# Optimization experiments

Hardware: AMD Instinct MI355X
Metric: run time of the kernel (lower is better)

The kernel has to match this reference:

```python
import jax, jax.numpy as jnp
import numpy as np

N_EXPERTS = 8
TOP_K = 2


def setup_inputs() -> dict:
    key = jax.random.key(0)
    ks = jax.random.split(key, 5)
    B, T, C, E, H = 8, 2048, 256, 8, 682  # H = int(8/3*256)
    scale = 1.0 / np.sqrt(C)
    return {
        "x": jax.random.normal(ks[0], (B, T, C), dtype=jnp.float32),
        "router_w": jax.random.normal(ks[1], (E, C), dtype=jnp.float32) * scale,
        "w1": jax.random.normal(ks[2], (E, H, C), dtype=jnp.float32) * scale,
        "w2": jax.random.normal(ks[3], (E, C, H), dtype=jnp.float32) * (1.0 / np.sqrt(H)),
        "w3": jax.random.normal(ks[4], (E, H, C), dtype=jnp.float32) * scale,
    }


def reference(x, router_w, w1, w2, w3):
    B, T, C = x.shape
    flat = x.reshape(-1, C)  # [N, C]

    # Router: softmax over experts, top-k selection, renormalize.
    logits = flat @ router_w.T                     # [N, E]
    probs = jax.nn.softmax(logits, axis=-1)
    topk_probs, topk_idx = jax.lax.top_k(probs, TOP_K)
    topk_probs = topk_probs / (jnp.sum(topk_probs, axis=-1, keepdims=True) + 1e-9)

    # Dense gate matrix [N, E]: zero for non-selected experts (same math as
    # the masked loop, since unselected experts contribute weight 0).
    onehot = jax.nn.one_hot(topk_idx, N_EXPERTS, dtype=flat.dtype)  # [N, K, E]
    gates = jnp.einsum("nk,nke->ne", topk_probs, onehot)           # [N, E]

    # SwiGLU experts, computed densely over E and combined with gates.
    h1 = jnp.einsum("nc,ehc->neh", flat, w1)       # [N, E, H]
    h3 = jnp.einsum("nc,ehc->neh", flat, w3)       # [N, E, H]
    h = jax.nn.silu(h1) * h3                       # [N, E, H]
    y = jnp.einsum("neh,ech->nec", h, w2)          # [N, E, C]
    out = jnp.einsum("ne,nec->nc", gates, y)       # [N, C]
    return out.reshape(B, T, C)
```

## Files before the change

kernel.cpp:

```cpp
#include <hip/hip_runtime.h>
#include <hip/hip_bf16.h>

#define N_TOK 16384
#define C_DIM 256
#define E_NUM 8
#define H_DIM 682
#define H_PAD 768
#define NROWS (N_TOK * 2)
#define HB 64
#define APB (NROWS / HB)

typedef short short8 __attribute__((ext_vector_type(8)));
typedef float floatx4 __attribute__((ext_vector_type(4)));
typedef unsigned int uint;

__device__ inline unsigned short f2bf(float v) {
    union { float f; uint u; } x; x.f = v;
    uint r = (x.u + 0x7fffu + ((x.u >> 16) & 1u)) >> 16;
    return (unsigned short)r;
}
__device__ inline float bf2f(unsigned short v) {
    union { uint u; float f; } x; x.u = ((uint)v) << 16; return x.f;
}

__device__ __forceinline__ void load_lds16(const void* g, void* l) {
    __builtin_amdgcn_global_load_lds(
        (const __attribute__((address_space(1))) unsigned int*)g,
        (__attribute__((address_space(3))) unsigned int*)l, 16, 0, 0);
}

#define P13 (E_NUM * H_PAD * (C_DIM / 2))
#define P2  (E_NUM * C_DIM * (H_PAD / 2))
__global__ void wconvert(const float* __restrict__ w1, const float* __restrict__ w3,
                         const float* __restrict__ w2, unsigned short* __restrict__ w1b,
                         unsigned short* __restrict__ w3b, unsigned short* __restrict__ w2b) {
    int idx = blockIdx.x * 256 + threadIdx.x;
    if (idx < 2 * P13) {
        const float* src = (idx < P13) ? w1 : w3;
        unsigned short* dst = (idx < P13) ? w1b : w3b;
        int i = (idx < P13) ? idx : idx - P13;
        int e = i / (H_PAD * (C_DIM / 2));
        int rem = i - e * (H_PAD * (C_DIM / 2));
        int r = rem / (C_DIM / 2);
        int c2 = rem - r * (C_DIM / 2);
        uint v = 0;
        if (r < H_DIM) {
            const float2 f = *(const float2*)(src + ((size_t)e * H_DIM + r) * C_DIM + c2 * 2);
            v = (uint)f2bf(f.x) | ((uint)f2bf(f.y) << 16);
        }
        ((uint*)dst)[i] = v;
    } else if (idx < 2 * P13 + P2) {
        int i = idx - 2 * P13;
        int e = i / (C_DIM * (H_PAD / 2));
        int rem = i - e * (C_DIM * (H_PAD / 2));
        int r = rem / (H_PAD / 2);
        int c2 = rem - r * (H_PAD / 2);
        uint v = 0;
        if (c2 * 2 < H_DIM) {
            const float2 f = *(const float2*)(w2 + ((size_t)e * C_DIM + r) * H_DIM + c2 * 2);
            v = (uint)f2bf(f.x) | ((uint)f2bf(f.y) << 16);
        }
        ((uint*)w2b)[i] = v;
    }
}

__global__ __launch_bounds__(256) void router_kernel(
    const float* __restrict__ x, const float* __restrict__ rw,
    unsigned short* __restrict__ xb, int* __restrict__ as_e, float* __restrict__ as_gate) {
    __shared__ float rws[E_NUM * C_DIM];
    int tid = threadIdx.x;
    for (int i = tid; i < E_NUM * C_DIM; i += 256) rws[i] = rw[i];
    __syncthreads();
    int wave = tid >> 6, lane = tid & 63;
    int t = blockIdx.x * 4 + wave;
    const float4 xv = *(const float4*)(x + (size_t)t * C_DIM + lane * 4);
    uint2 pk;
    pk.x = (uint)f2bf(xv.x) | ((uint)f2bf(xv.y) << 16);
    pk.y = (uint)f2bf(xv.z) | ((uint)f2bf(xv.w) << 16);
    *(uint2*)(xb + (size_t)t * C_DIM + lane * 4) = pk;
    float p[E_NUM];
#pragma unroll
    for (int e = 0; e < E_NUM; e++) {
        const float* wr = &rws[e * C_DIM + lane * 4];
        p[e] = xv.x * wr[0] + xv.y * wr[1] + xv.z * wr[2] + xv.w * wr[3];
    }
#pragma unroll
    for (int off = 32; off >= 1; off >>= 1) {
#pragma unroll
        for (int e = 0; e < E_NUM; e++) p[e] += __shfl_down(p[e], off, 64);
    }
    if (lane == 0) {
        float m = p[0];
#pragma unroll
        for (int e = 1; e < E_NUM; e++) m = fmaxf(m, p[e]);
        float s = 0.f, q[E_NUM];
#pragma unroll
        for (int e = 0; e < E_NUM; e++) { q[e] = expf(p[e] - m); s += q[e]; }
#pragma unroll
        for (int e = 0; e < E_NUM; e++) q[e] /= s;
        int e0 = 0;
#pragma unroll
        for (int e = 1; e < E_NUM; e++) if (q[e] > q[e0]) e0 = e;
        int e1 = (e0 == 0) ? 1 : 0;
#pragma unroll
        for (int e = 0; e < E_NUM; e++) {
            if (e != e0 && q[e] > q[e1]) e1 = e;
        }
        float g0 = q[e0], g1 = q[e1];
        float denom = g0 + g1 + 1e-9f;
        g0 /= denom; g1 /= denom;
        as_e[t * 2] = e0; as_gate[t * 2] = g0;
        as_e[t * 2 + 1] = e1; as_gate[t * 2 + 1] = g1;
    }
}

__global__ __launch_bounds__(256) void hist_kernel(const int* __restrict__ as_e,
                                                   int* __restrict__ block_hist) {
    __shared__ int lh[E_NUM];
    int b = blockIdx.x, tid = threadIdx.x;
    if (tid < E_NUM) lh[tid] = 0;
    __syncthreads();
    for (int i = tid; i < APB; i += 256) atomicAdd(&lh[as_e[b * APB + i]], 1);
    __syncthreads();
    if (tid < E_NUM) block_hist[b * E_NUM + tid] = lh[tid];
}

__global__ void scan2_kernel(const int* __restrict__ block_hist, int* __restrict__ offsets,
                             int* __restrict__ block_base) {
    __shared__ int tot[E_NUM], off[E_NUM];
    int e = threadIdx.x;
    if (e < E_NUM) {
        int s = 0;
        for (int b = 0; b < HB; b++) s += block_hist[b * E_NUM + e];
        tot[e] = s;
    }
    __syncthreads();
    if (e == 0) {
        int acc = 0;
        for (int i = 0; i < E_NUM; i++) { off[i] = acc; offsets[i] = acc; acc += tot[i]; }
        offsets[E_NUM] = acc;
    }
    __syncthreads();
    if (e < E_NUM) {
        int acc = off[e];
        for (int b = 0; b < HB; b++) { block_base[b * E_NUM + e] = acc; acc += block_hist[b * E_NUM + e]; }
    }
}

__global__ __launch_bounds__(256) void scatter_kernel(
    const int* __restrict__ as_e, const int* __restrict__ block_base,
    int* __restrict__ row_token, int* __restrict__ as_row) {
    __shared__ int cur[E_NUM];
    int b = blockIdx.x, tid = threadIdx.x;
    if (tid < E_NUM) cur[tid] = block_base[b * E_NUM + tid];
    __syncthreads();
    for (int i = tid; i < APB; i += 256) {
        int a = b * APB + i;
        int e = as_e[a];
        int p = atomicAdd(&cur[e], 1);
        row_token[p] = a >> 1;
        as_row[a] = p;
    }
}

__global__ __launch_bounds__(256, 2) void expert_ffn1(
    const unsigned short* __restrict__ xb, const unsigned short* __restrict__ w1b,
    const unsigned short* __restrict__ w3b, const int* __restrict__ offsets,
    const int* __restrict__ row_token, unsigned short* __restrict__ h) {
    int e = blockIdx.x >> 6;
    int mt = blockIdx.x & 63;
    int c = blockIdx.y;
    int off0 = offsets[e], off1 = offsets[e + 1];
    int row0 = off0 + mt * 128;
    if (row0 >= off1) return;
    int mval = min(128, off1 - row0);

    __shared__ union {
        unsigned short buf[2][12288];
        unsigned short Hs[128 * 136];
    } sm;

    int tid = threadIdx.x, lane = tid & 63, w = tid >> 6;
    int wm = w & 1, wn = w >> 1;
    int ra = tid >> 2;
    int acol = (tid & 3) * 8;
    int tok0 = row_token[row0 + min(ra, mval - 1)];
    int tok1 = row_token[row0 + min(ra + 64, mval - 1)];
    const unsigned short* a0p = xb + (size_t)tok0 * C_DIM + acol;
    const unsigned short* a1p = xb + (size_t)tok1 * C_DIM + acol;
    const unsigned short* b1p0 = w1b + ((size_t)e * H_PAD + c * 128 + ra) * C_DIM + acol;
    const unsigned short* b1p1 = b1p0 + (size_t)64 * C_DIM;
    const unsigned short* b3p0 = w3b + ((size_t)e * H_PAD + c * 128 + ra) * C_DIM + acol;
    const unsigned short* b3p1 = b3p0 + (size_t)64 * C_DIM;

    int wofs = w * 512;
    auto stage = [&](int kt, int s) {
        int kb = kt * 32;
        unsigned short* base = sm.buf[s];
        load_lds16(a0p + kb, base + wofs);
        load_lds16(a1p + kb, base + 2048 + wofs);
        load_lds16(b1p0 + kb, base + 4096 + wofs);
        load_lds16(b1p1 + kb, base + 6144 + wofs);
        load_lds16(b3p0 + kb, base + 8192 + wofs);
        load_lds16(b3p1 + kb, base + 10240 + wofs);
    };

    int ko = (lane >> 4) * 8;
    int l15 = lane & 15;
    int arowf = wm * 64 + l15;
    int browf = wn * 64 + l15;
    int quad = lane >> 4;

    stage(0, 0);

    floatx4 acc1[4][4], acc3[4][4];
#pragma unroll
    for (int m = 0; m < 4; m++)
#pragma unroll
        for (int n = 0; n < 4; n++) {
            acc1[m][n] = (floatx4){0.f, 0.f, 0.f, 0.f};
            acc3[m][n] = (floatx4){0.f, 0.f, 0.f, 0.f};
        }

    for (int kt = 0; kt < 8; kt++) {
        __syncthreads();
        if (kt + 1 < 8) stage(kt + 1, (kt + 1) & 1);
        const unsigned short* cur = sm.buf[kt & 1];
        short8 af[4], b1f[4], b3f[4];
#pragma unroll
        for (int m = 0; m < 4; m++) af[m] = *(short8*)&cur[(arowf + m * 16) * 32 + ko];
#pragma unroll
        for (int n = 0; n < 4; n++) {
            b1f[n] = *(short8*)&cur[4096 + (browf + n * 16) * 32 + ko];
            b3f[n] = *(short8*)&cur[8192 + (browf + n * 16) * 32 + ko];
        }
#pragma unroll
        for (int m = 0; m < 4; m++)
#pragma unroll
            for (int n = 0; n < 4; n++) {
                acc1[m][n] = __builtin_amdgcn_mfma_f32_16x16x32_bf16(af[m], b1f[n], acc1[m][n], 0, 0, 0);
                acc3[m][n] = __builtin_amdgcn_mfma_f32_16x16x32_bf16(af[m], b3f[n], acc3[m][n], 0, 0, 0);
            }
    }
    __syncthreads();

#pragma unroll
    for (int m = 0; m < 4; m++)
#pragma unroll
        for (int n = 0; n < 4; n++)
#pragma unroll
            for (int r = 0; r < 4; r++) {
                float h1 = acc1[m][n][r], h3 = acc3[m][n][r];
                float sv = h1 / (1.0f + __expf(-h1)) * h3;
                sm.Hs[(wm * 64 + m * 16 + quad * 4 + r) * 136 + wn * 64 + n * 16 + l15] = f2bf(sv);
            }
    __syncthreads();
#pragma unroll
    for (int it = 0; it < 8; it++) {
        int s = it * 256 + tid;
        int row = s >> 4, c16 = s & 15;
        if (row < mval)
            *(int4*)(h + (size_t)(row0 + row) * H_PAD + c * 128 + c16 * 8) =
                *(int4*)&sm.Hs[row * 136 + c16 * 8];
    }
}

__global__ __launch_bounds__(256, 2) void expert_ffn2(
    const unsigned short* __restrict__ h, const unsigned short* __restrict__ w2b,
    const int* __restrict__ offsets, unsigned short* __restrict__ y) {
    int e = blockIdx.x >> 6;
    int mt = blockIdx.x & 63;
    int p = blockIdx.y;
    int off0 = offsets[e], off1 = offsets[e + 1];
    int row0 = off0 + mt * 128;
    if (row0 >= off1) return;
    int mval = min(128, off1 - row0);

    __shared__ union {
        unsigned short buf[2][8192];
        unsigned short Hs[128 * 136];
    } sm;

    int tid = threadIdx.x, lane = tid & 63, w = tid >> 6;
    int wm = w & 1, wn = w >> 1;
    int ra = tid >> 2;
    int acol = (tid & 3) * 8;
    const unsigned short* ap0 = h + (size_t)(row0 + ra) * H_PAD + acol;
    const unsigned short* ap1 = ap0 + (size_t)64 * H_PAD;
    const unsigned short* bp0 = w2b + ((size_t)e * C_DIM + p * 128 + ra) * H_PAD + acol;
    const unsigned short* bp1 = bp0 + (size_t)64 * H_PAD;

    int wofs = w * 512;
    auto stage = [&](int kt, int s) {
        int kb = kt * 32;
        unsigned short* base = sm.buf[s];
        load_lds16(ap0 + kb, base + wofs);
        load_lds16(ap1 + kb, base + 2048 + wofs);
        load_lds16(bp0 + kb, base + 4096 + wofs);
        load_lds16(bp1 + kb, base + 6144 + wofs);
    };

    int ko = (lane >> 4) * 8;
    int l15 = lane & 15;
    int arowf = wm * 64 + l15;
    int browf = wn * 64 + l15;
    int quad = lane >> 4;

    stage(0, 0);

    floatx4 acc[4][4];
#pragma unroll
    for (int m = 0; m < 4; m++)
#pragma unroll
        for (int n = 0; n < 4; n++) acc[m][n] = (floatx4){0.f, 0.f, 0.f, 0.f};

    for (int kt = 0; kt < H_PAD / 32; kt++) {
        __syncthreads();
        if (kt + 1 < H_PAD / 32) stage(kt + 1, (kt + 1) & 1);
        const unsigned short* cur = sm.buf[kt & 1];
        short8 af[4], bf[4];
#pragma unroll
        for (int m = 0; m < 4; m++) af[m] = *(short8*)&cur[(arowf + m * 16) * 32 + ko];
#pragma unroll
        for (int n = 0; n < 4; n++) bf[n] = *(short8*)&cur[4096 + (browf + n * 16) * 32 + ko];
#pragma unroll
        for (int m = 0; m < 4; m++)
#pragma unroll
            for (int n = 0; n < 4; n++)
                acc[m][n] = __builtin_amdgcn_mfma_f32_16x16x32_bf16(af[m], bf[n], acc[m][n], 0, 0, 0);
    }
    __syncthreads();

#pragma unroll
    for (int m = 0; m < 4; m++)
#pragma unroll
        for (int n = 0; n < 4; n++)
#pragma unroll
            for (int r = 0; r < 4; r++)
                sm.Hs[(wm * 64 + m * 16 + quad * 4 + r) * 136 + wn * 64 + n * 16 + l15] =
                    f2bf(acc[m][n][r]);
    __syncthreads();
#pragma unroll
    for (int it = 0; it < 8; it++) {
        int s = it * 256 + tid;
        int row = s >> 4, c16 = s & 15;
        if (row < mval)
            *(int4*)(y + (size_t)(row0 + row) * C_DIM + p * 128 + c16 * 8) =
                *(int4*)&sm.Hs[row * 136 + c16 * 8];
    }
}

__global__ __launch_bounds__(256) void combine_kernel(
    const unsigned short* __restrict__ y, const int* __restrict__ as_row,
    const float* __restrict__ as_gate, float* __restrict__ out) {
    int tid = threadIdx.x, lane = tid & 63;
    int t = blockIdx.x * 4 + (tid >> 6);
    int r0 = as_row[2 * t], r1 = as_row[2 * t + 1];
    float g0 = as_gate[2 * t], g1 = as_gate[2 * t + 1];
    uint2 a = *(const uint2*)(y + (size_t)r0 * C_DIM + lane * 4);
    uint2 b = *(const uint2*)(y + (size_t)r1 * C_DIM + lane * 4);
    float4 o;
    o.x = g0 * bf2f((unsigned short)(a.x & 0xffff)) + g1 * bf2f((unsigned short)(b.x & 0xffff));
    o.y = g0 * bf2f((unsigned short)(a.x >> 16)) + g1 * bf2f((unsigned short)(b.x >> 16));
    o.z = g0 * bf2f((unsigned short)(a.y & 0xffff)) + g1 * bf2f((unsigned short)(b.y & 0xffff));
    o.w = g0 * bf2f((unsigned short)(a.y >> 16)) + g1 * bf2f((unsigned short)(b.y >> 16));
    *(float4*)(out + (size_t)t * C_DIM + lane * 4) = o;
}

extern "C" void kernel_launch(void* const* d_in, const int* in_sizes, int n_in,
                              void* d_out, int out_size, void* d_ws, size_t ws_size,
                              hipStream_t stream) {
    const float* x = (const float*)d_in[0];
    const float* rw = (const float*)d_in[1];
    const float* w1 = (const float*)d_in[2];
    const float* w2 = (const float*)d_in[3];
    const float* w3 = (const float*)d_in[4];
    float* out = (float*)d_out;

    char* ws = (char*)d_ws;
    size_t o = 0;
    auto alloc = [&](size_t bytes) {
        void* p = ws + o;
        o = (o + bytes + 255) & ~(size_t)255;
        return p;
    };
    unsigned short* xb = (unsigned short*)alloc((size_t)N_TOK * C_DIM * 2);
    unsigned short* w1b = (unsigned short*)alloc((size_t)E_NUM * H_PAD * C_DIM * 2);
    unsigned short* w3b = (unsigned short*)alloc((size_t)E_NUM * H_PAD * C_DIM * 2);
    unsigned short* w2b = (unsigned short*)alloc((size_t)E_NUM * C_DIM * H_PAD * 2);
    unsigned short* hbuf = (unsigned short*)alloc((size_t)(NROWS + 128) * H_PAD * 2);
    unsigned short* ybuf = (unsigned short*)alloc((size_t)NROWS * C_DIM * 2);
    int* offsets = (int*)alloc((E_NUM + 1) * 4);
    int* as_e = (int*)alloc(NROWS * 4);
    float* as_gate = (float*)alloc(NROWS * 4);
    int* row_token = (int*)alloc(NROWS * 4);
    int* as_row = (int*)alloc(NROWS * 4);
    int* block_hist = (int*)alloc(HB * E_NUM * 4);
    int* block_base = (int*)alloc(HB * E_NUM * 4);

    wconvert<<<(2 * P13 + P2 + 255) / 256, 256, 0, stream>>>(w1, w3, w2, w1b, w3b, w2b);
    router_kernel<<<N_TOK / 4, 256, 0, stream>>>(x, rw, xb, as_e, as_gate);
    hist_kernel<<<HB, 256, 0, stream>>>(as_e, block_hist);
    scan2_kernel<<<1, 64, 0, stream>>>(block_hist, offsets, block_base);
    scatter_kernel<<<HB, 256, 0, stream>>>(as_e, block_base, row_token, as_row);

    expert_ffn1<<<dim3(E_NUM * 64, 6), 256, 0, stream>>>(xb, w1b, w3b, offsets, row_token, hbuf);
    expert_ffn2<<<dim3(E_NUM * 64, 2), 256, 0, stream>>>(hbuf, w2b, offsets, ybuf);
    combine_kernel<<<N_TOK / 4, 256, 0, stream>>>(ybuf, as_row, as_gate, out);
}
```

Before: 201.7 us.

## Triple-buffer expert GEMM K-loop with vmcnt waits, XOR swizzle, and MFMA priority

```diff
diff --git a/kernel.cpp b/kernel.cpp
--- a/kernel.cpp
+++ b/kernel.cpp
@@ -28,6 +28,10 @@
         (const __attribute__((address_space(1))) unsigned int*)g,
         (__attribute__((address_space(3))) unsigned int*)l, 16, 0, 0);
 }
+
+#define VMCNT6 asm volatile("s_waitcnt vmcnt(6)" ::: "memory")
+#define VMCNT4 asm volatile("s_waitcnt vmcnt(4)" ::: "memory")
+#define VMCNT0 asm volatile("s_waitcnt vmcnt(0)" ::: "memory")
 
 #define P13 (E_NUM * H_PAD * (C_DIM / 2))
 #define P2  (E_NUM * C_DIM * (H_PAD / 2))
@@ -176,14 +180,14 @@
     int mval = min(128, off1 - row0);
 
     __shared__ union {
-        unsigned short buf[2][12288];
+        unsigned short buf[3][12288];
         unsigned short Hs[128 * 136];
     } sm;
 
     int tid = threadIdx.x, lane = tid & 63, w = tid >> 6;
     int wm = w & 1, wn = w >> 1;
     int ra = tid >> 2;
-    int acol = (tid & 3) * 8;
+    int acol = (((tid & 3) ^ ((ra >> 1) & 3))) * 8;
     int tok0 = row_token[row0 + min(ra, mval - 1)];
     int tok1 = row_token[row0 + min(ra + 64, mval - 1)];
     const unsigned short* a0p = xb + (size_t)tok0 * C_DIM + acol;
@@ -194,9 +198,8 @@
     const unsigned short* b3p1 = b3p0 + (size_t)64 * C_DIM;
 
     int wofs = w * 512;
-    auto stage = [&](int kt, int s) {
+    auto stage = [&](int kt, unsigned short* base) {
         int kb = kt * 32;
-        unsigned short* base = sm.buf[s];
         load_lds16(a0p + kb, base + wofs);
         load_lds16(a1p + kb, base + 2048 + wofs);
         load_lds16(b1p0 + kb, base + 4096 + wofs);
@@ -205,13 +208,14 @@
         load_lds16(b3p1 + kb, base + 10240 + wofs);
     };
 
-    int ko = (lane >> 4) * 8;
+    int ko = ((lane >> 4) ^ ((lane >> 1) & 3)) * 8;
     int l15 = lane & 15;
     int arowf = wm * 64 + l15;
     int browf = wn * 64 + l15;
     int quad = lane >> 4;
 
-    stage(0, 0);
+    stage(0, sm.buf[0]);
+    stage(1, sm.buf[1]);
 
     floatx4 acc1[4][4], acc3[4][4];
 #pragma unroll
@@ -222,10 +226,12 @@
             acc3[m][n] = (floatx4){0.f, 0.f, 0.f, 0.f};
         }
 
+#pragma unroll
     for (int kt = 0; kt < 8; kt++) {
-        __syncthreads();
-        if (kt + 1 < 8) stage(kt + 1, (kt + 1) & 1);
-        const unsigned short* cur = sm.buf[kt & 1];
+        if (kt == 7) { VMCNT0; } else { VMCNT6; }
+        __builtin_amdgcn_s_barrier();
+        if (kt + 2 < 8) stage(kt + 2, sm.buf[(kt + 2) % 3]);
+        const unsigned short* cur = sm.buf[kt % 3];
         short8 af[4], b1f[4], b3f[4];
 #pragma unroll
         for (int m = 0; m < 4; m++) af[m] = *(short8*)&cur[(arowf + m * 16) * 32 + ko];
@@ -234,6 +240,7 @@
             b1f[n] = *(short8*)&cur[4096 + (browf + n * 16) * 32 + ko];
             b3f[n] = *(short8*)&cur[8192 + (browf + n * 16) * 32 + ko];
         }
+        __builtin_amdgcn_s_setprio(1);
 #pragma unroll
         for (int m = 0; m < 4; m++)
 #pragma unroll
@@ -241,6 +248,8 @@
                 acc1[m][n] = __builtin_amdgcn_mfma_f32_16x16x32_bf16(af[m], b1f[n], acc1[m][n], 0, 0, 0);
                 acc3[m][n] = __builtin_amdgcn_mfma_f32_16x16x32_bf16(af[m], b3f[n], acc3[m][n], 0, 0, 0);
             }
+        __builtin_amdgcn_s_setprio(0);
+        __builtin_amdgcn_s_barrier();
     }
     __syncthreads();
 
@@ -265,7 +274,7 @@
     }
 }
 
-__global__ __launch_bounds__(256, 2) void expert_ffn2(
+__global__ __launch_bounds__(256, 3) void expert_ffn2(
     const unsigned short* __restrict__ h, const unsigned short* __restrict__ w2b,
     const int* __restrict__ offsets, unsigned short* __restrict__ y) {
     int e = blockIdx.x >> 6;
@@ -277,36 +286,36 @@
     int mval = min(128, off1 - row0);
 
     __shared__ union {
-        unsigned short buf[2][8192];
+        unsigned short buf[3][8192];
         unsigned short Hs[128 * 136];
     } sm;
 
     int tid = threadIdx.x, lane = tid & 63, w = tid >> 6;
     int wm = w & 1, wn = w >> 1;
     int ra = tid >> 2;
-    int acol = (tid & 3) * 8;
+    int acol = (((tid & 3) ^ ((ra >> 1) & 3))) * 8;
     const unsigned short* ap0 = h + (size_t)(row0 + ra) * H_PAD + acol;
     const unsigned short* ap1 = ap0 + (size_t)64 * H_PAD;
     const unsigned short* bp0 = w2b + ((size_t)e * C_DIM + p * 128 + ra) * H_PAD + acol;
     const unsigned short* bp1 = bp0 + (size_t)64 * H_PAD;
 
     int wofs = w * 512;
-    auto stage = [&](int kt, int s) {
+    auto stage = [&](int kt, unsigned short* base) {
         int kb = kt * 32;
-        unsigned short* base = sm.buf[s];
         load_lds16(ap0 + kb, base + wofs);
         load_lds16(ap1 + kb, base + 2048 + wofs);
         load_lds16(bp0 + kb, base + 4096 + wofs);
         load_lds16(bp1 + kb, base + 6144 + wofs);
     };
 
-    int ko = (lane >> 4) * 8;
+    int ko = ((lane >> 4) ^ ((lane >> 1) & 3)) * 8;
     int l15 = lane & 15;
     int arowf = wm * 64 + l15;
     int browf = wn * 64 + l15;
     int quad = lane >> 4;
 
-    stage(0, 0);
+    stage(0, sm.buf[0]);
+    stage(1, sm.buf[1]);
 
     floatx4 acc[4][4];
 #pragma unroll
@@ -314,20 +323,25 @@
 #pragma unroll
         for (int n = 0; n < 4; n++) acc[m][n] = (floatx4){0.f, 0.f, 0.f, 0.f};
 
+#pragma unroll
     for (int kt = 0; kt < H_PAD / 32; kt++) {
-        __syncthreads();
-        if (kt + 1 < H_PAD / 32) stage(kt + 1, (kt + 1) & 1);
-        const unsigned short* cur = sm.buf[kt & 1];
+        if (kt == H_PAD / 32 - 1) { VMCNT0; } else { VMCNT4; }
+        __builtin_amdgcn_s_barrier();
+        if (kt + 2 < H_PAD / 32) stage(kt + 2, sm.buf[(kt + 2) % 3]);
+        const unsigned short* cur = sm.buf[kt % 3];
         short8 af[4], bf[4];
 #pragma unroll
         for (int m = 0; m < 4; m++) af[m] = *(short8*)&cur[(arowf + m * 16) * 32 + ko];
 #pragma unroll
         for (int n = 0; n < 4; n++) bf[n] = *(short8*)&cur[4096 + (browf + n * 16) * 32 + ko];
+        __builtin_amdgcn_s_setprio(1);
 #pragma unroll
         for (int m = 0; m < 4; m++)
 #pragma unroll
             for (int n = 0; n < 4; n++)
                 acc[m][n] = __builtin_amdgcn_mfma_f32_16x16x32_bf16(af[m], bf[n], acc[m][n], 0, 0, 0);
+        __builtin_amdgcn_s_setprio(0);
+        __builtin_amdgcn_s_barrier();
     }
     __syncthreads();
 
```

Result: faster. 194.8 us (-3.4%).
